# Optimization experiments

Hardware: AMD Instinct MI355X
Metric: run time of the kernel (lower is better)

The kernel has to match this reference:

```python
import jax, jax.numpy as jnp
import numpy as np

# ---- config (matches init_kwargs) ----
B, S, V = 8, 900, 11
H, NH, HD = 512, 8, 64          # hidden, heads, head_dim = H // NH
L = 2                            # num_layers
EXPANSION = 4.0
INNER = 1536                     # find_multiple(round(4.0 * 512 * 2/3), 256)
STEPS = 2                        # mcmc_num_steps
EPS = 1e-5                       # rms_norm_eps
THETA = 10000.0                  # rope_theta
ESCALE = float(np.sqrt(H))       # embed_scale = sqrt(hidden_size)
SCALE = 1.0 / float(np.sqrt(HD))


def rms_norm(x):
    return x * jax.lax.rsqrt(jnp.mean(x * x, axis=-1, keepdims=True) + EPS)


def rope_tables():
    inv_freq = 1.0 / (THETA ** (jnp.arange(0, HD, 2, dtype=jnp.float32) / HD))
    t = jnp.arange(S, dtype=jnp.float32)
    freqs = jnp.outer(t, inv_freq)                # (S, HD/2)
    emb = jnp.concatenate([freqs, freqs], axis=-1)  # (S, HD)
    return jnp.cos(emb), jnp.sin(emb)


def rotate_half(x):
    x1, x2 = jnp.split(x, 2, axis=-1)
    return jnp.concatenate([-x2, x1], axis=-1)


def apply_rope(q, k, cos, sin):
    cos = cos[None, :, None, :]  # (1,S,1,HD) broadcast over batch & heads
    sin = sin[None, :, None, :]
    return q * cos + rotate_half(q) * sin, k * cos + rotate_half(k) * sin


def block(h, qkv_w, o_w, gu_w, d_w, cos, sin):
    b, s, _ = h.shape
    qkv = (h @ qkv_w).reshape(b, s, 3 * NH, HD)
    q, k, v = qkv[:, :, :NH], qkv[:, :, NH:2 * NH], qkv[:, :, 2 * NH:]
    q, k = apply_rope(q, k, cos, sin)
    scores = jnp.einsum('bqhd,bkhd->bhqk', q, k) * SCALE
    attn = jax.nn.softmax(scores, axis=-1)
    out = jnp.einsum('bhqk,bkhd->bqhd', attn, v).reshape(b, s, NH * HD)
    h = rms_norm(h + out @ o_w)                   # post-norm residual
    gu = h @ gu_w
    gate, up = gu[..., :INNER], gu[..., INNER:]
    h = rms_norm(h + (jax.nn.silu(gate) * up) @ d_w)
    return h


def energy(logits, embed_w, energy_w, qkv_w, o_w, gu_w, d_w, input_emb, cos, sin):
    probs = jax.nn.softmax(logits, axis=-1)       # soft token distribution
    h = input_emb + ESCALE * (probs @ embed_w)    # soft embedding
    for i in range(L):
        h = block(h, qkv_w[i], o_w[i], gu_w[i], d_w[i], cos, sin)
    return jnp.sum(h @ energy_w)                  # scalar energy


def setup_inputs() -> dict:
    key = jax.random.key(0)
    ks = jax.random.split(key, 8)
    inputs = jax.random.randint(ks[0], (B, S), 0, V, dtype=jnp.int64)
    puzzle_identifiers = jax.random.randint(ks[1], (B,), 0, 1, dtype=jnp.int64)
    init_std = 1.0 / ESCALE
    embed_w = jax.random.normal(ks[2], (V, H), jnp.float32) * init_std
    energy_w = jax.random.normal(ks[3], (H, 1), jnp.float32) * 0.02
    qkv_w = jax.random.normal(ks[4], (L, H, 3 * NH * HD), jnp.float32) * 0.02
    o_w = jax.random.normal(ks[5], (L, NH * HD, H), jnp.float32) * 0.02
    gu_w = jax.random.normal(ks[6], (L, H, 2 * INNER), jnp.float32) * 0.02
    d_w = jax.random.normal(ks[7], (L, INNER, H), jnp.float32) * 0.02
    alpha = jnp.asarray(100.0, jnp.float32)       # mcmc_step_size
    return {"inputs": inputs, "puzzle_identifiers": puzzle_identifiers,
            "embed_w": embed_w, "energy_w": energy_w, "qkv_w": qkv_w,
            "o_w": o_w, "gu_w": gu_w, "d_w": d_w, "alpha": alpha}


def reference(inputs, puzzle_identifiers, embed_w, energy_w, qkv_w, o_w, gu_w, d_w, alpha):
    cos, sin = rope_tables()
    input_emb = ESCALE * embed_w[inputs]          # (B,S,H)
    a = jnp.maximum(alpha, 1e-4)                  # torch.clamp(alpha, min=1e-4)
    logits = jnp.zeros((inputs.shape[0], S, V), jnp.float32)
    egrad = jax.grad(energy)
    for _ in range(STEPS):                        # MCMC energy-descent loop
        g = egrad(logits, embed_w, energy_w, qkv_w, o_w, gu_w, d_w, input_emb, cos, sin)
        logits = logits - a * g
    return logits
```

## Files before the change

kernel.cpp:

```cpp
#include <hip/hip_runtime.h>
#include <math.h>

#define B_ 8
#define S_ 900
#define V_ 11
#define H_ 512
#define NH_ 8
#define HD_ 64
#define INNER_ 1536
#define STEPS_ 2
#define NTOK (B_*S_)
#define EPS_ 1e-5f
#define THETA_ 10000.0f
#define ESCALE_ 22.627416997969522f
#define SCALE_ 0.125f
#define PT_ 68

typedef __attribute__((ext_vector_type(8))) short bh8;
typedef __attribute__((ext_vector_type(4))) float f32x4;
typedef __attribute__((ext_vector_type(4))) unsigned short us4;

union bfu { bh8 v; unsigned short s[8]; us4 q[2]; };

__device__ inline unsigned short f2bf(float x) {
  unsigned u = __builtin_bit_cast(unsigned, x);
  return (unsigned short)((u + 0x7FFFu + ((u >> 16) & 1u)) >> 16);
}
__device__ inline float b2f(unsigned short s) {
  return __builtin_bit_cast(float, (unsigned)s << 16);
}

__device__ inline void gld16(const unsigned short* g, unsigned short* l) {
  __builtin_amdgcn_global_load_lds(
      (const __attribute__((address_space(1))) void*)(g),
      (__attribute__((address_space(3))) void*)(l), 16, 0, 0);
}

__device__ inline bh8 lds16(const unsigned short* p) {
  bfu u;
  u.q[0] = *(const us4*)p;
  u.q[1] = *(const us4*)(p + 4);
  return u.v;
}
__device__ inline void sts16(unsigned short* p, bfu u) {
  *(us4*)p = u.q[0];
  *(us4*)(p + 4) = u.q[1];
}

__device__ inline float wave_sum64(float x) {
#pragma unroll
  for (int off = 32; off > 0; off >>= 1) x += __shfl_xor(x, off, 64);
  return x;
}

__device__ inline float quad_sum(float x) {
  x += __shfl_xor(x, 1, 64);
  x += __shfl_xor(x, 2, 64);
  return x;
}


__global__ void k_zero(float* p, int n) {
  int i = blockIdx.x * blockDim.x + threadIdx.x;
  if (i < n) p[i] = 0.f;
}

__global__ void k_rope_tables(float* cs, float* sn) {
  int idx = blockIdx.x * blockDim.x + threadIdx.x;
  if (idx >= S_ * 32) return;
  int s = idx >> 5, i = idx & 31;
  float freq = powf(THETA_, -(float)i / 32.0f);
  float ang = (float)s * freq;
  cs[idx] = cosf(ang);
  sn[idx] = sinf(ang);
}

__global__ void k_softmax_logits(const float* __restrict__ logits, float* __restrict__ P) {
  int t = blockIdx.x * blockDim.x + threadIdx.x;
  if (t >= NTOK) return;
  float x[V_];
  float m = -1e30f;
#pragma unroll
  for (int v = 0; v < V_; ++v) { x[v] = logits[t * V_ + v]; m = fmaxf(m, x[v]); }
  float ssum = 0.f;
#pragma unroll
  for (int v = 0; v < V_; ++v) { x[v] = expf(x[v] - m); ssum += x[v]; }
  float inv = 1.f / ssum;
#pragma unroll
  for (int v = 0; v < V_; ++v) P[t * V_ + v] = x[v] * inv;
}

__global__ void k_h0(const float* __restrict__ P, const float* __restrict__ E,
                     const int* __restrict__ inp, float* __restrict__ h0,
                     unsigned short* __restrict__ h016) {
  int t = blockIdx.x;
  int tid = threadIdx.x;
  __shared__ float p[V_];
  __shared__ int iw;
  if (tid < V_) p[tid] = P[t * V_ + tid];
  if (tid == 0) iw = inp[t];
  __syncthreads();
  for (int h = tid; h < H_; h += blockDim.x) {
    float acc = E[iw * H_ + h];
#pragma unroll
    for (int v = 0; v < V_; ++v) acc += p[v] * E[v * H_ + h];
    float val = ESCALE_ * acc;
    h0[(size_t)t * H_ + h] = val;
    h016[(size_t)t * H_ + h] = f2bf(val);
  }
}

__global__ void k_gfill(const float* __restrict__ ew, float* __restrict__ G) {
  int idx = blockIdx.x * blockDim.x + threadIdx.x;
  if (idx < NTOK * H_) G[idx] = ew[idx & (H_ - 1)];
}

__global__ void k_cast8(const float* __restrict__ X, unsigned short* __restrict__ Y, int n8) {
  int i = blockIdx.x * blockDim.x + threadIdx.x;
  if (i >= n8) return;
  const float4* p = (const float4*)(X + (size_t)i * 8);
  float4 a = p[0], b = p[1];
  bfu o;
  o.s[0] = f2bf(a.x); o.s[1] = f2bf(a.y); o.s[2] = f2bf(a.z); o.s[3] = f2bf(a.w);
  o.s[4] = f2bf(b.x); o.s[5] = f2bf(b.y); o.s[6] = f2bf(b.z); o.s[7] = f2bf(b.w);
  *(bh8*)(Y + (size_t)i * 8) = o.v;
}


__global__ void k_wt(const float* __restrict__ W, unsigned short* __restrict__ WT, int K, int N) {
  __shared__ float t[32][33];
  int k0 = blockIdx.y * 32, n0 = blockIdx.x * 32;
  int tx = threadIdx.x, ty = threadIdx.y;
#pragma unroll
  for (int i = 0; i < 4; ++i)
    t[ty + 8 * i][tx] = W[(size_t)(k0 + ty + 8 * i) * N + n0 + tx];
  __syncthreads();
#pragma unroll
  for (int i = 0; i < 4; ++i)
    WT[(size_t)(n0 + ty + 8 * i) * K + k0 + tx] = f2bf(t[tx][ty + 8 * i]);
}


template <int SILU_A, int ADD, int CBF, int ROPE, int SILUBWD>
__global__ __launch_bounds__(256) void k_gemm(const unsigned short* __restrict__ A16,
                                              const unsigned short* __restrict__ Bt,
                                              const float* __restrict__ Dm,
                                              float* __restrict__ Cf,
                                              unsigned short* __restrict__ C16,
                                              unsigned short* __restrict__ GU,
                                              const float* __restrict__ Cs,
                                              const float* __restrict__ Sn,
                                              int M, int N, int K, int lda) {
  __shared__ unsigned short As[64][32];
  __shared__ unsigned short Bs[128][32];
  int tid = threadIdx.x;
  int m0 = blockIdx.y * 64, n0 = blockIdx.x * 128;
  int wid = tid >> 6, lane = tid & 63;
  int wr = (wid >> 1) * 32, wc = (wid & 1) * 64;
  int lr = lane & 15, lg = lane >> 4;
  int srow = lane >> 2, sck = (lane & 3) * 8;
  f32x4 acc[2][4] = {};
  for (int k0 = 0; k0 < K; k0 += 32) {
    __syncthreads();
    if (SILU_A) {
      int row = tid >> 2, ck = (tid & 3) * 8;
      int gr = m0 + row; gr = gr < M ? gr : M - 1;
      const unsigned short* src = &A16[(size_t)gr * lda + k0 + ck];
      bfu pa;
#pragma unroll
      for (int j = 0; j < 8; ++j) {
        float g = b2f(src[j]), u = b2f(src[INNER_ + j]);
        pa.s[j] = f2bf((g / (1.f + __expf(-g))) * u);
      }
      *(bh8*)&As[row][ck] = pa.v;
    } else {
      int row = wid * 16 + srow;
      int gr = m0 + row; gr = gr < M ? gr : M - 1;
      gld16(&A16[(size_t)gr * lda + k0 + sck], &As[wid * 16][0]);
    }
#pragma unroll
    for (int i = 0; i < 2; ++i) {
      int bb = wid * 2 + i;
      gld16(&Bt[(size_t)(n0 + bb * 16 + srow) * K + k0 + sck], &Bs[bb * 16][0]);
    }
    __syncthreads();
    bh8 av[2], bv[4];
#pragma unroll
    for (int fr = 0; fr < 2; ++fr) av[fr] = *(const bh8*)&As[wr + fr * 16 + lr][lg * 8];
#pragma unroll
    for (int fc = 0; fc < 4; ++fc) bv[fc] = *(const bh8*)&Bs[wc + fc * 16 + lr][lg * 8];
#pragma unroll
    for (int fr = 0; fr < 2; ++fr)
#pragma unroll
      for (int fc = 0; fc < 4; ++fc)
        acc[fr][fc] = __builtin_amdgcn_mfma_f32_16x16x32_bf16(av[fr], bv[fc], acc[fr][fc], 0, 0, 0);
  }
  bool rope_on = ROPE && (((n0 + wc) >> 6) < 16);
#pragma unroll
  for (int fr = 0; fr < 2; ++fr) {
    int r0 = m0 + wr + fr * 16 + lg * 4;
#pragma unroll
    for (int i = 0; i < 4; ++i) {
      int gr = r0 + i;
      if (gr >= M) continue;
      float c0 = 1.f, s0 = 0.f, c1 = 1.f, s1 = 0.f;
      if (ROPE) {
        if (rope_on) {
          int s = gr % S_;
          c0 = Cs[s * 32 + lr];      s0 = Sn[s * 32 + lr];
          c1 = Cs[s * 32 + 16 + lr]; s1 = Sn[s * 32 + 16 + lr];
        }
      }
#pragma unroll
      for (int fc = 0; fc < 4; ++fc) {
        int gc = n0 + wc + fc * 16 + lr;
        float out = acc[fr][fc][i];
        if (ROPE) {
          float part = acc[fr][fc ^ 2][i];
          float cc = (fc & 1) ? c1 : c0;
          float ss = (fc & 1) ? s1 : s0;
          out = (fc < 2) ? (out * cc - part * ss) : (out * cc + part * ss);
        }
        if (ADD) out += Dm[(size_t)gr * N + gc];
        if (SILUBWD) {
          size_t gb = (size_t)gr * (size_t)(2 * INNER_) + gc;
          float g = b2f(GU[gb]), u = b2f(GU[gb + INNER_]);
          float sig = 1.f / (1.f + __expf(-g));
          GU[gb] = f2bf(out * u * sig * (1.f + g * (1.f - sig)));
          GU[gb + INNER_] = f2bf(out * g * sig);
        } else if (CBF) {
          C16[(size_t)gr * N + gc] = f2bf(out);
        } else {
          Cf[(size_t)gr * N + gc] = out;
        }
      }
    }
  }
}


__global__ __launch_bounds__(256) void k_attn_fwd3(const unsigned short* __restrict__ QKV,
                                                   unsigned short* __restrict__ AO,
                                                   float* __restrict__ MB,
                                                   float* __restrict__ LB) {
  __shared__ unsigned short Ks[64][PT_];
  __shared__ unsigned short VT[64][PT_];
  __shared__ unsigned short Ps[4][16][PT_];
  int tid = threadIdx.x;
  int h = blockIdx.y, b = blockIdx.z;
  int w = tid >> 6, lane = tid & 63;
  int lr = lane & 15, lg = lane >> 4;
  int q0 = blockIdx.x * 64 + w * 16;

  bh8 qf[2];
  {
    int qr = q0 + lr; if (qr >= S_) qr = S_ - 1;
    const unsigned short* qp = &QKV[((size_t)(b * S_ + qr) * 24 + h) * 64 + lg * 8];
    qf[0] = *(const bh8*)qp;
    qf[1] = *(const bh8*)(qp + 32);
  }
  f32x4 accO[4] = {};
  float m[4], lsum[4];
#pragma unroll
  for (int i = 0; i < 4; ++i) { m[i] = -1e30f; lsum[i] = 0.f; }

  for (int kt = 0; kt < S_; kt += 64) {
    __syncthreads();
    {
      int r = tid >> 2, c0 = (tid & 3) * 16;
      int src = kt + r;
      size_t ts = (size_t)b * S_ + (src < S_ ? src : S_ - 1);
      const unsigned short* gp = &QKV[(ts * 24 + 8 + h) * 64 + c0];
      bfu p0, p1;
      p0.v = *(const bh8*)gp;
      p1.v = *(const bh8*)(gp + 8);
      sts16(&Ks[r][c0], p0);
      sts16(&Ks[r][c0 + 8], p1);
    }
    {
      int d0 = (tid & 15) * 4, k0r = (tid >> 4) * 4;
      us4 rv[4];
#pragma unroll
      for (int j = 0; j < 4; ++j) {
        int src = kt + k0r + j;
        size_t ts = (size_t)b * S_ + (src < S_ ? src : S_ - 1);
        rv[j] = *(const us4*)&QKV[(ts * 24 + 16 + h) * 64 + d0];
      }
#pragma unroll
      for (int dd = 0; dd < 4; ++dd) {
        us4 pk = {rv[0][dd], rv[1][dd], rv[2][dd], rv[3][dd]};
        *(us4*)&VT[d0 + dd][k0r] = pk;
      }
    }
    __syncthreads();
    f32x4 accS[4] = {};
#pragma unroll
    for (int ks = 0; ks < 2; ++ks)
#pragma unroll
      for (int fk = 0; fk < 4; ++fk)
        accS[fk] = __builtin_amdgcn_mfma_f32_16x16x32_bf16(qf[ks], lds16(&Ks[fk * 16 + lr][ks * 32 + lg * 8]), accS[fk], 0, 0, 0);
    float sc[4][4], pmax[4];
#pragma unroll
    for (int i = 0; i < 4; ++i) pmax[i] = -1e30f;
#pragma unroll
    for (int fk = 0; fk < 4; ++fk)
#pragma unroll
      for (int i = 0; i < 4; ++i) {
        float s = accS[fk][i] * SCALE_;
        if (kt + fk * 16 + lr >= S_) s = -1e30f;
        sc[fk][i] = s;
        pmax[i] = fmaxf(pmax[i], s);
      }
#pragma unroll
    for (int i = 0; i < 4; ++i) {
      float v = pmax[i];
      v = fmaxf(v, __shfl_xor(v, 1, 64));
      v = fmaxf(v, __shfl_xor(v, 2, 64));
      v = fmaxf(v, __shfl_xor(v, 4, 64));
      v = fmaxf(v, __shfl_xor(v, 8, 64));
      pmax[i] = v;
    }
    float psum[4];
#pragma unroll
    for (int i = 0; i < 4; ++i) {
      float mn = fmaxf(m[i], pmax[i]);
      float eo = __expf(m[i] - mn);
      m[i] = mn;
      lsum[i] *= eo;
#pragma unroll
      for (int fd = 0; fd < 4; ++fd) accO[fd][i] *= eo;
      psum[i] = 0.f;
    }
#pragma unroll
    for (int fk = 0; fk < 4; ++fk)
#pragma unroll
      for (int i = 0; i < 4; ++i) {
        float p = __expf(sc[fk][i] - m[i]);
        sc[fk][i] = p;
        psum[i] += p;
      }
#pragma unroll
    for (int i = 0; i < 4; ++i) {
      float v = psum[i];
      v += __shfl_xor(v, 1, 64);
      v += __shfl_xor(v, 2, 64);
      v += __shfl_xor(v, 4, 64);
      v += __shfl_xor(v, 8, 64);
      lsum[i] += v;
    }
#pragma unroll
    for (int fk = 0; fk < 4; ++fk)
#pragma unroll
      for (int i = 0; i < 4; ++i)
        Ps[w][lg * 4 + i][fk * 16 + lr] = f2bf(sc[fk][i]);
#pragma unroll
    for (int ks = 0; ks < 2; ++ks) {
      bh8 ap = lds16(&Ps[w][lr][ks * 32 + lg * 8]);
#pragma unroll
      for (int fd = 0; fd < 4; ++fd)
        accO[fd] = __builtin_amdgcn_mfma_f32_16x16x32_bf16(ap, lds16(&VT[fd * 16 + lr][ks * 32 + lg * 8]), accO[fd], 0, 0, 0);
    }
  }
#pragma unroll
  for (int i = 0; i < 4; ++i) {
    int q = q0 + lg * 4 + i;
    if (q < S_) {
      float linv = 1.f / lsum[i];
      size_t obase = (size_t)(b * S_ + q) * H_ + h * 64;
#pragma unroll
      for (int fd = 0; fd < 4; ++fd) AO[obase + fd * 16 + lr] = f2bf(accO[fd][i] * linv);
      if (lr == 0) {
        MB[((size_t)b * NH_ + h) * S_ + q] = m[i];
        LB[((size_t)b * NH_ + h) * S_ + q] = linv;
      }
    }
  }
}

__global__ __launch_bounds__(256) void k_delta(const unsigned short* __restrict__ O,
                                               const unsigned short* __restrict__ dO,
                                               float* __restrict__ DB) {
  int tid = threadIdx.x;
  int h = blockIdx.y, b = blockIdx.z;
  int r = blockIdx.x * 64 + (tid >> 2), part = tid & 3;
  if (r >= S_) return;
  size_t base = (size_t)(b * S_ + r) * H_ + h * 64 + part * 16;
  bfu o0, o1, d0, d1;
  o0.v = *(const bh8*)&O[base];  o1.v = *(const bh8*)&O[base + 8];
  d0.v = *(const bh8*)&dO[base]; d1.v = *(const bh8*)&dO[base + 8];
  float s = 0.f;
#pragma unroll
  for (int j = 0; j < 8; ++j)
    s += b2f(o0.s[j]) * b2f(d0.s[j]) + b2f(o1.s[j]) * b2f(d1.s[j]);
  s = quad_sum(s);
  if (part == 0) DB[((size_t)b * NH_ + h) * S_ + r] = s;
}

__global__ __launch_bounds__(256) void k_attn_bwd_dq3(const unsigned short* __restrict__ QKV,
                                                      const unsigned short* __restrict__ dO,
                                                      const float* __restrict__ MB,
                                                      const float* __restrict__ LB,
                                                      const float* __restrict__ DB,
                                                      const float* __restrict__ Cs,
                                                      const float* __restrict__ Sn,
                                                      unsigned short* __restrict__ dQKV) {
  __shared__ unsigned short Ks[64][PT_];
  __shared__ unsigned short Vs[64][PT_];
  __shared__ unsigned short KT[64][PT_];
  __shared__ unsigned short Ps[4][16][PT_];
  int tid = threadIdx.x;
  int h = blockIdx.y, b = blockIdx.z;
  int w = tid >> 6, lane = tid & 63;
  int lr = lane & 15, lg = lane >> 4;
  int q0 = blockIdx.x * 64 + w * 16;
  size_t sbase = ((size_t)b * NH_ + h) * S_;

  bh8 qf[2], dof[2];
  {
    int qr = q0 + lr; if (qr >= S_) qr = S_ - 1;
    const unsigned short* qp = &QKV[((size_t)(b * S_ + qr) * 24 + h) * 64 + lg * 8];
    const unsigned short* dp = &dO[(size_t)(b * S_ + qr) * H_ + h * 64 + lg * 8];
    qf[0] = *(const bh8*)qp;  qf[1] = *(const bh8*)(qp + 32);
    dof[0] = *(const bh8*)dp; dof[1] = *(const bh8*)(dp + 32);
  }
  float mrow[4], lrow[4], drow[4];
#pragma unroll
  for (int i = 0; i < 4; ++i) {
    int q = q0 + lg * 4 + i; if (q >= S_) q = S_ - 1;
    mrow[i] = MB[sbase + q];
    lrow[i] = LB[sbase + q];
    drow[i] = DB[sbase + q];
  }
  f32x4 accQ[4] = {};

  for (int kt = 0; kt < S_; kt += 64) {
    __syncthreads();
    {
      int r = tid >> 2, c0 = (tid & 3) * 16;
      int src = kt + r;
      bool vld = src < S_;
      size_t ts = (size_t)b * S_ + (vld ? src : S_ - 1);
      const unsigned short* kp = &QKV[(ts * 24 + 8 + h) * 64 + c0];
      bfu p0{}, p1{}, p2{}, p3{};
      if (vld) {
        p0.v = *(const bh8*)kp;
        p1.v = *(const bh8*)(kp + 8);
        p2.v = *(const bh8*)(kp + 512);
        p3.v = *(const bh8*)(kp + 520);
      }
      sts16(&Ks[r][c0], p0); sts16(&Ks[r][c0 + 8], p1);
      sts16(&Vs[r][c0], p2); sts16(&Vs[r][c0 + 8], p3);
    }
    {
      int d0 = (tid & 15) * 4, k0r = (tid >> 4) * 4;
      us4 rv[4];
#pragma unroll
      for (int j = 0; j < 4; ++j) {
        int src = kt + k0r + j;
        bool vld = src < S_;
        size_t ts = (size_t)b * S_ + (vld ? src : S_ - 1);
        us4 t = *(const us4*)&QKV[(ts * 24 + 8 + h) * 64 + d0];
        if (!vld) t = us4{0, 0, 0, 0};
        rv[j] = t;
      }
#pragma unroll
      for (int dd = 0; dd < 4; ++dd) {
        us4 pk = {rv[0][dd], rv[1][dd], rv[2][dd], rv[3][dd]};
        *(us4*)&KT[d0 + dd][k0r] = pk;
      }
    }
    __syncthreads();
    f32x4 aS[4] = {}, aD[4] = {};
#pragma unroll
    for (int ks = 0; ks < 2; ++ks)
#pragma unroll
      for (int fk = 0; fk < 4; ++fk) {
        aS[fk] = __builtin_amdgcn_mfma_f32_16x16x32_bf16(qf[ks], lds16(&Ks[fk * 16 + lr][ks * 32 + lg * 8]), aS[fk], 0, 0, 0);
        aD[fk] = __builtin_amdgcn_mfma_f32_16x16x32_bf16(dof[ks], lds16(&Vs[fk * 16 + lr][ks * 32 + lg * 8]), aD[fk], 0, 0, 0);
      }
#pragma unroll
    for (int fk = 0; fk < 4; ++fk)
#pragma unroll
      for (int i = 0; i < 4; ++i) {
        float p = __expf(aS[fk][i] * SCALE_ - mrow[i]) * lrow[i];
        float ds = p * (aD[fk][i] - drow[i]);
        Ps[w][lg * 4 + i][fk * 16 + lr] = f2bf(ds);
      }
#pragma unroll
    for (int ks = 0; ks < 2; ++ks) {
      bh8 ap = lds16(&Ps[w][lr][ks * 32 + lg * 8]);
#pragma unroll
      for (int fd = 0; fd < 4; ++fd)
        accQ[fd] = __builtin_amdgcn_mfma_f32_16x16x32_bf16(ap, lds16(&KT[fd * 16 + lr][ks * 32 + lg * 8]), accQ[fd], 0, 0, 0);
    }
  }
#pragma unroll
  for (int i = 0; i < 4; ++i) {
    int q = q0 + lg * 4 + i;
    if (q < S_) {
      size_t obase = ((size_t)(b * S_ + q) * 24 + h) * 64;
      float c0 = Cs[q * 32 + lr], s0 = Sn[q * 32 + lr];
      float c1 = Cs[q * 32 + 16 + lr], s1 = Sn[q * 32 + 16 + lr];
#pragma unroll
      for (int fd = 0; fd < 4; ++fd) {
        float x = SCALE_ * accQ[fd][i];
        float p = SCALE_ * accQ[fd ^ 2][i];
        float cc = (fd & 1) ? c1 : c0;
        float ss = (fd & 1) ? s1 : s0;
        float out = (fd < 2) ? (x * cc + p * ss) : (x * cc - p * ss);
        dQKV[obase + fd * 16 + lr] = f2bf(out);
      }
    }
  }
}

__global__ __launch_bounds__(256) void k_attn_bwd_kv3(const unsigned short* __restrict__ QKV,
                                                      const unsigned short* __restrict__ dO,
                                                      const float* __restrict__ MB,
                                                      const float* __restrict__ LB,
                                                      const float* __restrict__ DB,
                                                      const float* __restrict__ Cs,
                                                      const float* __restrict__ Sn,
                                                      unsigned short* __restrict__ dQKV) {
  __shared__ unsigned short Qs[64][PT_];
  __shared__ unsigned short dOs[64][PT_];
  __shared__ unsigned short QT[64][PT_];
  __shared__ unsigned short dOT[64][PT_];
  __shared__ unsigned short Ps[4][16][PT_];
  __shared__ float sM[64], sL[64], sD[64];
  int tid = threadIdx.x;
  int h = blockIdx.y, b = blockIdx.z;
  int w = tid >> 6, lane = tid & 63;
  int lr = lane & 15, lg = lane >> 4;
  int k0w = blockIdx.x * 64 + w * 16;
  size_t sbase = ((size_t)b * NH_ + h) * S_;

  bh8 kf[2], vf[2];
  {
    int kr = k0w + lr; if (kr >= S_) kr = S_ - 1;
    const unsigned short* kp = &QKV[((size_t)(b * S_ + kr) * 24 + 8 + h) * 64 + lg * 8];
    kf[0] = *(const bh8*)kp;        kf[1] = *(const bh8*)(kp + 32);
    vf[0] = *(const bh8*)(kp + 512); vf[1] = *(const bh8*)(kp + 544);
  }
  f32x4 accK[4] = {}, accV[4] = {};

  for (int qt = 0; qt < S_; qt += 64) {
    __syncthreads();
    {
      int r = tid >> 2, c0 = (tid & 3) * 16;
      int src = qt + r;
      bool vld = src < S_;
      size_t ts = (size_t)b * S_ + (vld ? src : S_ - 1);
      const unsigned short* qp = &QKV[(ts * 24 + h) * 64 + c0];
      const unsigned short* dp = &dO[ts * H_ + h * 64 + c0];
      bfu p0, p1, p2{}, p3{};
      p0.v = *(const bh8*)qp;
      p1.v = *(const bh8*)(qp + 8);
      if (vld) {
        p2.v = *(const bh8*)dp;
        p3.v = *(const bh8*)(dp + 8);
      }
      sts16(&Qs[r][c0], p0);  sts16(&Qs[r][c0 + 8], p1);
      sts16(&dOs[r][c0], p2); sts16(&dOs[r][c0 + 8], p3);
    }
    {
      int d0 = (tid & 15) * 4, q0r = (tid >> 4) * 4;
      us4 rq[4], rd[4];
#pragma unroll
      for (int j = 0; j < 4; ++j) {
        int src = qt + q0r + j;
        bool vld = src < S_;
        size_t ts = (size_t)b * S_ + (vld ? src : S_ - 1);
        rq[j] = *(const us4*)&QKV[(ts * 24 + h) * 64 + d0];
        us4 td = *(const us4*)&dO[ts * H_ + h * 64 + d0];
        if (!vld) td = us4{0, 0, 0, 0};
        rd[j] = td;
      }
#pragma unroll
      for (int dd = 0; dd < 4; ++dd) {
        us4 pq = {rq[0][dd], rq[1][dd], rq[2][dd], rq[3][dd]};
        us4 pd = {rd[0][dd], rd[1][dd], rd[2][dd], rd[3][dd]};
        *(us4*)&QT[d0 + dd][q0r] = pq;
        *(us4*)&dOT[d0 + dd][q0r] = pd;
      }
    }
    if (tid < 64) {
      int src = qt + tid;
      bool vld = src < S_;
      int sc = vld ? src : S_ - 1;
      sM[tid] = MB[sbase + sc];
      sL[tid] = LB[sbase + sc];
      sD[tid] = vld ? DB[sbase + sc] : 0.f;
    }
    __syncthreads();
    f32x4 aS[4] = {}, aD[4] = {};
#pragma unroll
    for (int ks = 0; ks < 2; ++ks)
#pragma unroll
      for (int fq = 0; fq < 4; ++fq) {
        aS[fq] = __builtin_amdgcn_mfma_f32_16x16x32_bf16(kf[ks], lds16(&Qs[fq * 16 + lr][ks * 32 + lg * 8]), aS[fq], 0, 0, 0);
        aD[fq] = __builtin_amdgcn_mfma_f32_16x16x32_bf16(vf[ks], lds16(&dOs[fq * 16 + lr][ks * 32 + lg * 8]), aD[fq], 0, 0, 0);
      }
    float pv[4][4];
#pragma unroll
    for (int fq = 0; fq < 4; ++fq) {
      float mq = sM[fq * 16 + lr], lq = sL[fq * 16 + lr];
#pragma unroll
      for (int i = 0; i < 4; ++i) {
        float p = __expf(aS[fq][i] * SCALE_ - mq) * lq;
        pv[fq][i] = p;
        Ps[w][lg * 4 + i][fq * 16 + lr] = f2bf(p);
      }
    }
#pragma unroll
    for (int qs = 0; qs < 2; ++qs) {
      bh8 ap = lds16(&Ps[w][lr][qs * 32 + lg * 8]);
#pragma unroll
      for (int fd = 0; fd < 4; ++fd)
        accV[fd] = __builtin_amdgcn_mfma_f32_16x16x32_bf16(ap, lds16(&dOT[fd * 16 + lr][qs * 32 + lg * 8]), accV[fd], 0, 0, 0);
    }
#pragma unroll
    for (int fq = 0; fq < 4; ++fq) {
      float dq = sD[fq * 16 + lr];
#pragma unroll
      for (int i = 0; i < 4; ++i)
        Ps[w][lg * 4 + i][fq * 16 + lr] = f2bf(pv[fq][i] * (aD[fq][i] - dq));
    }
#pragma unroll
    for (int qs = 0; qs < 2; ++qs) {
      bh8 ap = lds16(&Ps[w][lr][qs * 32 + lg * 8]);
#pragma unroll
      for (int fd = 0; fd < 4; ++fd)
        accK[fd] = __builtin_amdgcn_mfma_f32_16x16x32_bf16(ap, lds16(&QT[fd * 16 + lr][qs * 32 + lg * 8]), accK[fd], 0, 0, 0);
    }
  }
#pragma unroll
  for (int i = 0; i < 4; ++i) {
    int k = k0w + lg * 4 + i;
    if (k < S_) {
      size_t obase = ((size_t)(b * S_ + k) * 24 + 8 + h) * 64;
      float c0 = Cs[k * 32 + lr], s0 = Sn[k * 32 + lr];
      float c1 = Cs[k * 32 + 16 + lr], s1 = Sn[k * 32 + 16 + lr];
#pragma unroll
      for (int fd = 0; fd < 4; ++fd) {
        float x = SCALE_ * accK[fd][i];
        float p = SCALE_ * accK[fd ^ 2][i];
        float cc = (fd & 1) ? c1 : c0;
        float ss = (fd & 1) ? s1 : s0;
        float out = (fd < 2) ? (x * cc + p * ss) : (x * cc - p * ss);
        dQKV[obase + fd * 16 + lr] = f2bf(out);
        dQKV[obase + 512 + fd * 16 + lr] = f2bf(accV[fd][i]);
      }
    }
  }
}


__global__ __launch_bounds__(256) void k_rms_fwd(const float* __restrict__ X, float* __restrict__ Y,
                                                 unsigned short* __restrict__ Y16) {
  int t = blockIdx.x, tid = threadIdx.x;
  float x0 = X[(size_t)t * H_ + tid], x1 = X[(size_t)t * H_ + tid + 256];
  __shared__ float red[256];
  red[tid] = x0 * x0 + x1 * x1;
  __syncthreads();
  for (int s = 128; s > 0; s >>= 1) {
    if (tid < s) red[tid] += red[tid + s];
    __syncthreads();
  }
  float r = rsqrtf(red[0] / H_ + EPS_);
  float y0 = x0 * r, y1 = x1 * r;
  Y[(size_t)t * H_ + tid] = y0;
  Y[(size_t)t * H_ + tid + 256] = y1;
  Y16[(size_t)t * H_ + tid] = f2bf(y0);
  Y16[(size_t)t * H_ + tid + 256] = f2bf(y1);
}

__global__ __launch_bounds__(256) void k_rms_bwd(const float* __restrict__ X,
                                                 const float* __restrict__ GY,
                                                 float* __restrict__ GX,
                                                 unsigned short* __restrict__ GX16) {
  int t = blockIdx.x, tid = threadIdx.x;
  float x0 = X[(size_t)t * H_ + tid], x1 = X[(size_t)t * H_ + tid + 256];
  float g0 = GY[(size_t)t * H_ + tid], g1 = GY[(size_t)t * H_ + tid + 256];
  __shared__ float r1[256], r2[256];
  r1[tid] = x0 * x0 + x1 * x1;
  r2[tid] = x0 * g0 + x1 * g1;
  __syncthreads();
  for (int s = 128; s > 0; s >>= 1) {
    if (tid < s) { r1[tid] += r1[tid + s]; r2[tid] += r2[tid + s]; }
    __syncthreads();
  }
  float r = rsqrtf(r1[0] / H_ + EPS_);
  float coef = r * r * r * r2[0] / (float)H_;
  float o0 = r * g0 - coef * x0, o1 = r * g1 - coef * x1;
  GX[(size_t)t * H_ + tid] = o0;
  GX[(size_t)t * H_ + tid + 256] = o1;
  GX16[(size_t)t * H_ + tid] = f2bf(o0);
  GX16[(size_t)t * H_ + tid + 256] = f2bf(o1);
}


__global__ __launch_bounds__(64) void k_logits_update(const float* __restrict__ G,
                                                      const float* __restrict__ E,
                                                      const float* __restrict__ P,
                                                      const float* __restrict__ alpha,
                                                      float* __restrict__ logits) {
  int t = blockIdx.x, lane = threadIdx.x;
  float dp[V_];
#pragma unroll
  for (int v = 0; v < V_; ++v) dp[v] = 0.f;
  for (int hh = lane; hh < H_; hh += 64) {
    float gh = G[(size_t)t * H_ + hh];
#pragma unroll
    for (int v = 0; v < V_; ++v) dp[v] += gh * E[v * H_ + hh];
  }
#pragma unroll
  for (int v = 0; v < V_; ++v) dp[v] = wave_sum64(dp[v]) * ESCALE_;
  float dot = 0.f;
  float pv[V_];
#pragma unroll
  for (int v = 0; v < V_; ++v) {
    pv[v] = P[t * V_ + v];
    dot += pv[v] * dp[v];
  }
  float a = fmaxf(alpha[0], 1e-4f);
  if (lane < V_) logits[t * V_ + lane] -= a * pv[lane] * (dp[lane] - dot);
}


struct Ctx {
  unsigned short *Q16, *Q016, *dQ16, *GU16, *DO16, *AO16, *AO016, *X116, *UDX16;
  float *X1, *X2, *G, *UDX, *P, *MB, *LB, *DB, *MB0, *LB0, *CS, *SN;
  const unsigned short *WTqkv[2], *WTo[2], *WTgu[2], *WTd[2];
  const unsigned short *WSqkv[2], *WSo[2], *WSgu[2], *WSd[2];
  hipStream_t st;
};

static inline dim3 ggrid(int M, int N) { return dim3(N / 128, (M + 63) / 64); }

static void block_forward(Ctx& c, int l, const float* hin, const unsigned short* hin16,
                          float* hout, unsigned short* qb, unsigned short* ao,
                          float* mb, float* lb, bool skip_attn) {
  if (!skip_attn) {
    k_gemm<0, 0, 1, 1, 0><<<ggrid(NTOK, 3 * H_), 256, 0, c.st>>>(
        hin16, c.WTqkv[l], nullptr, nullptr, qb, nullptr, c.CS, c.SN, NTOK, 3 * H_, H_, H_);
    k_attn_fwd3<<<dim3((S_ + 63) / 64, NH_, B_), 256, 0, c.st>>>(qb, ao, mb, lb);
  }
  k_gemm<0, 1, 0, 0, 0><<<ggrid(NTOK, H_), 256, 0, c.st>>>(
      ao, c.WTo[l], hin, c.X1, nullptr, nullptr, nullptr, nullptr, NTOK, H_, H_, H_);
  k_rms_fwd<<<NTOK, 256, 0, c.st>>>(c.X1, c.UDX, c.UDX16);
  k_gemm<0, 0, 1, 0, 0><<<ggrid(NTOK, 2 * INNER_), 256, 0, c.st>>>(
      c.UDX16, c.WTgu[l], nullptr, nullptr, c.GU16, nullptr, nullptr, nullptr, NTOK, 2 * INNER_, H_, H_);
  k_gemm<1, 1, 0, 0, 0><<<ggrid(NTOK, H_), 256, 0, c.st>>>(
      c.GU16, c.WTd[l], c.UDX, c.X2, nullptr, nullptr, nullptr, nullptr, NTOK, H_, INNER_, 2 * INNER_);
  if (hout) k_rms_fwd<<<NTOK, 256, 0, c.st>>>(c.X2, hout, c.UDX16);
}

static void block_backward(Ctx& c, int l, const float* hin, const unsigned short* hin16,
                           unsigned short* qb, unsigned short* ao, float* mb, float* lb,
                           bool skip_attn) {
  block_forward(c, l, hin, hin16, nullptr, qb, ao, mb, lb, skip_attn);
  k_rms_bwd<<<NTOK, 256, 0, c.st>>>(c.X2, c.G, c.UDX, c.UDX16);
  k_gemm<0, 0, 0, 0, 1><<<ggrid(NTOK, INNER_), 256, 0, c.st>>>(
      c.UDX16, c.WSd[l], nullptr, nullptr, nullptr, c.GU16, nullptr, nullptr, NTOK, INNER_, H_, H_);
  k_gemm<0, 1, 0, 0, 0><<<ggrid(NTOK, H_), 256, 0, c.st>>>(
      c.GU16, c.WSgu[l], c.UDX, c.G, nullptr, nullptr, nullptr, nullptr, NTOK, H_, 2 * INNER_, 2 * INNER_);
  k_rms_bwd<<<NTOK, 256, 0, c.st>>>(c.X1, c.G, c.UDX, c.UDX16);
  k_gemm<0, 0, 1, 0, 0><<<ggrid(NTOK, H_), 256, 0, c.st>>>(
      c.UDX16, c.WSo[l], nullptr, nullptr, c.DO16, nullptr, nullptr, nullptr, NTOK, H_, H_, H_);
  dim3 agrid((S_ + 63) / 64, NH_, B_);
  k_delta<<<agrid, 256, 0, c.st>>>(ao, c.DO16, c.DB);
  k_attn_bwd_dq3<<<agrid, 256, 0, c.st>>>(qb, c.DO16, mb, lb, c.DB, c.CS, c.SN, c.dQ16);
  k_attn_bwd_kv3<<<agrid, 256, 0, c.st>>>(qb, c.DO16, mb, lb, c.DB, c.CS, c.SN, c.dQ16);
  k_gemm<0, 1, 0, 0, 0><<<ggrid(NTOK, H_), 256, 0, c.st>>>(
      c.dQ16, c.WSqkv[l], c.UDX, c.G, nullptr, nullptr, nullptr, nullptr, NTOK, H_, 3 * H_, 3 * H_);
}

extern "C" void kernel_launch(void* const* d_in, const int* in_sizes, int n_in,
                              void* d_out, int out_size, void* d_ws, size_t ws_size,
                              hipStream_t stream) {
  const int* inputs = (const int*)d_in[0];
  const float* E = (const float*)d_in[2];
  const float* ew = (const float*)d_in[3];
  const float* qkvw = (const float*)d_in[4];
  const float* ow = (const float*)d_in[5];
  const float* guw = (const float*)d_in[6];
  const float* dw = (const float*)d_in[7];
  const float* alpha = (const float*)d_in[8];
  float* logits = (float*)d_out;

  const size_t WT_FLOATS = 3407872;
  const size_t NEED =
      3 * ((size_t)NTOK * 3 * H_ / 2) +
      ((size_t)NTOK * INNER_) +
      4 * ((size_t)NTOK * H_) +
      5 * ((size_t)NTOK * H_ / 2) +
      ((size_t)NTOK * V_) +
      5 * ((size_t)B_ * NH_ * S_) +
      2 * ((size_t)S_ * 32) +
      2 * WT_FLOATS;
  if (ws_size < NEED * sizeof(float)) {
    k_zero<<<(NTOK * V_ + 255) / 256, 256, 0, stream>>>(logits, NTOK * V_);
    return;
  }

  float* f = (float*)d_ws;
  Ctx c;
  c.st = stream;
  c.Q16 = (unsigned short*)f;  f += (size_t)NTOK * 3 * H_ / 2;
  c.Q016 = (unsigned short*)f; f += (size_t)NTOK * 3 * H_ / 2;
  c.dQ16 = (unsigned short*)f; f += (size_t)NTOK * 3 * H_ / 2;
  c.GU16 = (unsigned short*)f; f += (size_t)NTOK * INNER_;
  c.X1 = f;   f += (size_t)NTOK * H_;
  c.X2 = f;   f += (size_t)NTOK * H_;
  c.G = f;    f += (size_t)NTOK * H_;
  c.UDX = f;  f += (size_t)NTOK * H_;
  c.AO16 = (unsigned short*)f;  f += (size_t)NTOK * H_ / 2;
  c.AO016 = (unsigned short*)f; f += (size_t)NTOK * H_ / 2;
  c.DO16 = (unsigned short*)f;  f += (size_t)NTOK * H_ / 2;
  c.X116 = (unsigned short*)f;  f += (size_t)NTOK * H_ / 2;
  c.UDX16 = (unsigned short*)f; f += (size_t)NTOK * H_ / 2;
  c.P = f;    f += (size_t)NTOK * V_;
  c.MB = f;   f += (size_t)B_ * NH_ * S_;
  c.LB = f;   f += (size_t)B_ * NH_ * S_;
  c.DB = f;   f += (size_t)B_ * NH_ * S_;
  c.MB0 = f;  f += (size_t)B_ * NH_ * S_;
  c.LB0 = f;  f += (size_t)B_ * NH_ * S_;
  c.CS = f;   f += (size_t)S_ * 32;
  c.SN = f;   f += (size_t)S_ * 32;
  unsigned short* wt = (unsigned short*)f;

  const size_t LQKV = (size_t)H_ * 3 * H_;
  const size_t LO = (size_t)H_ * H_;
  const size_t LGU = (size_t)H_ * 2 * INNER_;
  const size_t LD = (size_t)INNER_ * H_;

  for (int l = 0; l < 2; ++l) {
    c.WTqkv[l] = wt;
    k_wt<<<dim3(3 * H_ / 32, H_ / 32), dim3(32, 8), 0, stream>>>(qkvw + l * LQKV, wt, H_, 3 * H_);
    wt += LQKV;
    c.WTo[l] = wt;
    k_wt<<<dim3(H_ / 32, H_ / 32), dim3(32, 8), 0, stream>>>(ow + l * LO, wt, H_, H_);
    wt += LO;
    c.WTgu[l] = wt;
    k_wt<<<dim3(2 * INNER_ / 32, H_ / 32), dim3(32, 8), 0, stream>>>(guw + l * LGU, wt, H_, 2 * INNER_);
    wt += LGU;
    c.WTd[l] = wt;
    k_wt<<<dim3(H_ / 32, INNER_ / 32), dim3(32, 8), 0, stream>>>(dw + l * LD, wt, INNER_, H_);
    wt += LD;
  }
  {
    unsigned short* ws = wt;
    k_cast8<<<(int)((2 * LQKV / 8 + 255) / 256), 256, 0, stream>>>(qkvw, ws, (int)(2 * LQKV / 8));
    c.WSqkv[0] = ws; c.WSqkv[1] = ws + LQKV; ws += 2 * LQKV;
    k_cast8<<<(int)((2 * LO / 8 + 255) / 256), 256, 0, stream>>>(ow, ws, (int)(2 * LO / 8));
    c.WSo[0] = ws; c.WSo[1] = ws + LO; ws += 2 * LO;
    k_cast8<<<(int)((2 * LGU / 8 + 255) / 256), 256, 0, stream>>>(guw, ws, (int)(2 * LGU / 8));
    c.WSgu[0] = ws; c.WSgu[1] = ws + LGU; ws += 2 * LGU;
    k_cast8<<<(int)((2 * LD / 8 + 255) / 256), 256, 0, stream>>>(dw, ws, (int)(2 * LD / 8));
    c.WSd[0] = ws; c.WSd[1] = ws + LD;
  }

  k_zero<<<(NTOK * V_ + 255) / 256, 256, 0, stream>>>(logits, NTOK * V_);
  k_rope_tables<<<(S_ * 32 + 255) / 256, 256, 0, stream>>>(c.CS, c.SN);

  for (int step = 0; step < STEPS_; ++step) {
    k_softmax_logits<<<(NTOK + 255) / 256, 256, 0, stream>>>(logits, c.P);
    k_h0<<<NTOK, 256, 0, stream>>>(c.P, E, inputs, c.X1, c.X116);
    block_forward(c, 0, c.X1, c.X116, c.UDX, c.Q016, c.AO016, c.MB0, c.LB0, false);
    k_gfill<<<(NTOK * H_ + 255) / 256, 256, 0, stream>>>(ew, c.G);
    block_backward(c, 1, c.UDX, c.UDX16, c.Q16, c.AO16, c.MB, c.LB, false);
    k_h0<<<NTOK, 256, 0, stream>>>(c.P, E, inputs, c.X1, c.X116);
    block_backward(c, 0, c.X1, c.X116, c.Q016, c.AO016, c.MB0, c.LB0, true);
    k_logits_update<<<NTOK, 64, 0, stream>>>(c.G, E, c.P, alpha, logits);
  }
}
```

Baseline: 2.635 ms.

## Add 128-row GEMM tiles and cache layer-0 forward activations for backward recompute

Adds a TM template parameter to the bf16 MFMA GEMM so the wide-N GEMMs (QKV, gate/up, SiLU-backward) use 128x128 tiles for more reuse per block. Layer 0's forward now keeps its post-MLP residual (X20) and normalized bf16 input (U016). Layer 0's backward therefore skips the rms_fwd and down-projection recompute. The O-projection and gate/up GEMMs are still rerun, since X1 and GU16 get overwritten by layer 1. This costs two extra workspace buffers and more accumulator registers per thread in the 128-row tiles.

```diff
diff --git a/kernel.cpp b/kernel.cpp
--- a/kernel.cpp
+++ b/kernel.cpp
@@ -141,7 +141,7 @@
 }
 
 
-template <int SILU_A, int ADD, int CBF, int ROPE, int SILUBWD>
+template <int TM, int SILU_A, int ADD, int CBF, int ROPE, int SILUBWD>
 __global__ __launch_bounds__(256) void k_gemm(const unsigned short* __restrict__ A16,
                                               const unsigned short* __restrict__ Bt,
                                               const float* __restrict__ Dm,
@@ -151,32 +151,36 @@
                                               const float* __restrict__ Cs,
                                               const float* __restrict__ Sn,
                                               int M, int N, int K, int lda) {
-  __shared__ unsigned short As[64][32];
+  __shared__ unsigned short As[TM][32];
   __shared__ unsigned short Bs[128][32];
+  constexpr int FR = TM / 32;
   int tid = threadIdx.x;
-  int m0 = blockIdx.y * 64, n0 = blockIdx.x * 128;
+  int m0 = blockIdx.y * TM, n0 = blockIdx.x * 128;
   int wid = tid >> 6, lane = tid & 63;
-  int wr = (wid >> 1) * 32, wc = (wid & 1) * 64;
+  int wr = (wid >> 1) * (FR * 16), wc = (wid & 1) * 64;
   int lr = lane & 15, lg = lane >> 4;
   int srow = lane >> 2, sck = (lane & 3) * 8;
-  f32x4 acc[2][4] = {};
+  f32x4 acc[FR][4] = {};
   for (int k0 = 0; k0 < K; k0 += 32) {
     __syncthreads();
-    if (SILU_A) {
-      int row = tid >> 2, ck = (tid & 3) * 8;
-      int gr = m0 + row; gr = gr < M ? gr : M - 1;
-      const unsigned short* src = &A16[(size_t)gr * lda + k0 + ck];
-      bfu pa;
-#pragma unroll
-      for (int j = 0; j < 8; ++j) {
-        float g = b2f(src[j]), u = b2f(src[INNER_ + j]);
-        pa.s[j] = f2bf((g / (1.f + __expf(-g))) * u);
-      }
-      *(bh8*)&As[row][ck] = pa.v;
-    } else {
-      int row = wid * 16 + srow;
-      int gr = m0 + row; gr = gr < M ? gr : M - 1;
-      gld16(&A16[(size_t)gr * lda + k0 + sck], &As[wid * 16][0]);
+#pragma unroll
+    for (int half = 0; half < TM / 64; ++half) {
+      if (SILU_A) {
+        int row = (tid >> 2) + 64 * half;
+        int ck = (tid & 3) * 8;
+        int gr = m0 + row; gr = gr < M ? gr : M - 1;
+        const unsigned short* src = &A16[(size_t)gr * lda + k0 + ck];
+        bfu pa;
+#pragma unroll
+        for (int j = 0; j < 8; ++j) {
+          float g = b2f(src[j]), u = b2f(src[INNER_ + j]);
+          pa.s[j] = f2bf((g / (1.f + __expf(-g))) * u);
+        }
+        *(bh8*)&As[row][ck] = pa.v;
+      } else {
+        int gr = m0 + 64 * half + wid * 16 + srow; gr = gr < M ? gr : M - 1;
+        gld16(&A16[(size_t)gr * lda + k0 + sck], &As[64 * half + wid * 16][0]);
+      }
     }
 #pragma unroll
     for (int i = 0; i < 2; ++i) {
@@ -184,20 +188,20 @@
       gld16(&Bt[(size_t)(n0 + bb * 16 + srow) * K + k0 + sck], &Bs[bb * 16][0]);
     }
     __syncthreads();
-    bh8 av[2], bv[4];
-#pragma unroll
-    for (int fr = 0; fr < 2; ++fr) av[fr] = *(const bh8*)&As[wr + fr * 16 + lr][lg * 8];
+    bh8 av[FR], bv[4];
+#pragma unroll
+    for (int fr = 0; fr < FR; ++fr) av[fr] = *(const bh8*)&As[wr + fr * 16 + lr][lg * 8];
 #pragma unroll
     for (int fc = 0; fc < 4; ++fc) bv[fc] = *(const bh8*)&Bs[wc + fc * 16 + lr][lg * 8];
 #pragma unroll
-    for (int fr = 0; fr < 2; ++fr)
+    for (int fr = 0; fr < FR; ++fr)
 #pragma unroll
       for (int fc = 0; fc < 4; ++fc)
         acc[fr][fc] = __builtin_amdgcn_mfma_f32_16x16x32_bf16(av[fr], bv[fc], acc[fr][fc], 0, 0, 0);
   }
   bool rope_on = ROPE && (((n0 + wc) >> 6) < 16);
 #pragma unroll
-  for (int fr = 0; fr < 2; ++fr) {
+  for (int fr = 0; fr < FR; ++fr) {
     int r0 = m0 + wr + fr * 16 + lg * 4;
 #pragma unroll
     for (int i = 0; i < 4; ++i) {
@@ -729,50 +733,56 @@
 
 
 struct Ctx {
-  unsigned short *Q16, *Q016, *dQ16, *GU16, *DO16, *AO16, *AO016, *X116, *UDX16;
-  float *X1, *X2, *G, *UDX, *P, *MB, *LB, *DB, *MB0, *LB0, *CS, *SN;
+  unsigned short *Q16, *Q016, *dQ16, *GU16, *DO16, *AO16, *AO016, *X116, *UDX16, *U016;
+  float *X1, *X2, *X20, *G, *UDX, *P, *MB, *LB, *DB, *MB0, *LB0, *CS, *SN;
   const unsigned short *WTqkv[2], *WTo[2], *WTgu[2], *WTd[2];
   const unsigned short *WSqkv[2], *WSo[2], *WSgu[2], *WSd[2];
   hipStream_t st;
 };
 
-static inline dim3 ggrid(int M, int N) { return dim3(N / 128, (M + 63) / 64); }
-
 static void block_forward(Ctx& c, int l, const float* hin, const unsigned short* hin16,
                           float* hout, unsigned short* qb, unsigned short* ao,
-                          float* mb, float* lb, bool skip_attn) {
-  if (!skip_attn) {
-    k_gemm<0, 0, 1, 1, 0><<<ggrid(NTOK, 3 * H_), 256, 0, c.st>>>(
-        hin16, c.WTqkv[l], nullptr, nullptr, qb, nullptr, c.CS, c.SN, NTOK, 3 * H_, H_, H_);
-    k_attn_fwd3<<<dim3((S_ + 63) / 64, NH_, B_), 256, 0, c.st>>>(qb, ao, mb, lb);
-  }
-  k_gemm<0, 1, 0, 0, 0><<<ggrid(NTOK, H_), 256, 0, c.st>>>(
+                          float* mb, float* lb, float* x2buf, unsigned short* u16buf) {
+  k_gemm<128, 0, 0, 1, 1, 0><<<dim3(3 * H_ / 128, (NTOK + 127) / 128), 256, 0, c.st>>>(
+      hin16, c.WTqkv[l], nullptr, nullptr, qb, nullptr, c.CS, c.SN, NTOK, 3 * H_, H_, H_);
+  k_attn_fwd3<<<dim3((S_ + 63) / 64, NH_, B_), 256, 0, c.st>>>(qb, ao, mb, lb);
+  k_gemm<64, 0, 1, 0, 0, 0><<<dim3(H_ / 128, (NTOK + 63) / 64), 256, 0, c.st>>>(
       ao, c.WTo[l], hin, c.X1, nullptr, nullptr, nullptr, nullptr, NTOK, H_, H_, H_);
-  k_rms_fwd<<<NTOK, 256, 0, c.st>>>(c.X1, c.UDX, c.UDX16);
-  k_gemm<0, 0, 1, 0, 0><<<ggrid(NTOK, 2 * INNER_), 256, 0, c.st>>>(
-      c.UDX16, c.WTgu[l], nullptr, nullptr, c.GU16, nullptr, nullptr, nullptr, NTOK, 2 * INNER_, H_, H_);
-  k_gemm<1, 1, 0, 0, 0><<<ggrid(NTOK, H_), 256, 0, c.st>>>(
-      c.GU16, c.WTd[l], c.UDX, c.X2, nullptr, nullptr, nullptr, nullptr, NTOK, H_, INNER_, 2 * INNER_);
-  if (hout) k_rms_fwd<<<NTOK, 256, 0, c.st>>>(c.X2, hout, c.UDX16);
+  k_rms_fwd<<<NTOK, 256, 0, c.st>>>(c.X1, c.UDX, u16buf);
+  k_gemm<128, 0, 0, 1, 0, 0><<<dim3(2 * INNER_ / 128, (NTOK + 127) / 128), 256, 0, c.st>>>(
+      u16buf, c.WTgu[l], nullptr, nullptr, c.GU16, nullptr, nullptr, nullptr, NTOK, 2 * INNER_, H_, H_);
+  k_gemm<64, 1, 1, 0, 0, 0><<<dim3(H_ / 128, (NTOK + 63) / 64), 256, 0, c.st>>>(
+      c.GU16, c.WTd[l], c.UDX, x2buf, nullptr, nullptr, nullptr, nullptr, NTOK, H_, INNER_, 2 * INNER_);
+  if (hout) k_rms_fwd<<<NTOK, 256, 0, c.st>>>(x2buf, hout, c.UDX16);
 }
 
 static void block_backward(Ctx& c, int l, const float* hin, const unsigned short* hin16,
                            unsigned short* qb, unsigned short* ao, float* mb, float* lb,
-                           bool skip_attn) {
-  block_forward(c, l, hin, hin16, nullptr, qb, ao, mb, lb, skip_attn);
-  k_rms_bwd<<<NTOK, 256, 0, c.st>>>(c.X2, c.G, c.UDX, c.UDX16);
-  k_gemm<0, 0, 0, 0, 1><<<ggrid(NTOK, INNER_), 256, 0, c.st>>>(
+                           bool full) {
+  const float* x2src;
+  if (full) {
+    block_forward(c, l, hin, hin16, nullptr, qb, ao, mb, lb, c.X2, c.UDX16);
+    x2src = c.X2;
+  } else {
+    k_gemm<64, 0, 1, 0, 0, 0><<<dim3(H_ / 128, (NTOK + 63) / 64), 256, 0, c.st>>>(
+        ao, c.WTo[l], hin, c.X1, nullptr, nullptr, nullptr, nullptr, NTOK, H_, H_, H_);
+    k_gemm<128, 0, 0, 1, 0, 0><<<dim3(2 * INNER_ / 128, (NTOK + 127) / 128), 256, 0, c.st>>>(
+        c.U016, c.WTgu[l], nullptr, nullptr, c.GU16, nullptr, nullptr, nullptr, NTOK, 2 * INNER_, H_, H_);
+    x2src = c.X20;
+  }
+  k_rms_bwd<<<NTOK, 256, 0, c.st>>>(x2src, c.G, c.UDX, c.UDX16);
+  k_gemm<128, 0, 0, 0, 0, 1><<<dim3(INNER_ / 128, (NTOK + 127) / 128), 256, 0, c.st>>>(
       c.UDX16, c.WSd[l], nullptr, nullptr, nullptr, c.GU16, nullptr, nullptr, NTOK, INNER_, H_, H_);
-  k_gemm<0, 1, 0, 0, 0><<<ggrid(NTOK, H_), 256, 0, c.st>>>(
+  k_gemm<64, 0, 1, 0, 0, 0><<<dim3(H_ / 128, (NTOK + 63) / 64), 256, 0, c.st>>>(
       c.GU16, c.WSgu[l], c.UDX, c.G, nullptr, nullptr, nullptr, nullptr, NTOK, H_, 2 * INNER_, 2 * INNER_);
   k_rms_bwd<<<NTOK, 256, 0, c.st>>>(c.X1, c.G, c.UDX, c.UDX16);
-  k_gemm<0, 0, 1, 0, 0><<<ggrid(NTOK, H_), 256, 0, c.st>>>(
+  k_gemm<64, 0, 0, 1, 0, 0><<<dim3(H_ / 128, (NTOK + 63) / 64), 256, 0, c.st>>>(
       c.UDX16, c.WSo[l], nullptr, nullptr, c.DO16, nullptr, nullptr, nullptr, NTOK, H_, H_, H_);
   dim3 agrid((S_ + 63) / 64, NH_, B_);
   k_delta<<<agrid, 256, 0, c.st>>>(ao, c.DO16, c.DB);
   k_attn_bwd_dq3<<<agrid, 256, 0, c.st>>>(qb, c.DO16, mb, lb, c.DB, c.CS, c.SN, c.dQ16);
   k_attn_bwd_kv3<<<agrid, 256, 0, c.st>>>(qb, c.DO16, mb, lb, c.DB, c.CS, c.SN, c.dQ16);
-  k_gemm<0, 1, 0, 0, 0><<<ggrid(NTOK, H_), 256, 0, c.st>>>(
+  k_gemm<64, 0, 1, 0, 0, 0><<<dim3(H_ / 128, (NTOK + 63) / 64), 256, 0, c.st>>>(
       c.dQ16, c.WSqkv[l], c.UDX, c.G, nullptr, nullptr, nullptr, nullptr, NTOK, H_, 3 * H_, 3 * H_);
 }
 
@@ -793,8 +803,8 @@
   const size_t NEED =
       3 * ((size_t)NTOK * 3 * H_ / 2) +
       ((size_t)NTOK * INNER_) +
-      4 * ((size_t)NTOK * H_) +
-      5 * ((size_t)NTOK * H_ / 2) +
+      5 * ((size_t)NTOK * H_) +
+      6 * ((size_t)NTOK * H_ / 2) +
       ((size_t)NTOK * V_) +
       5 * ((size_t)B_ * NH_ * S_) +
       2 * ((size_t)S_ * 32) +
@@ -813,6 +823,7 @@
   c.GU16 = (unsigned short*)f; f += (size_t)NTOK * INNER_;
   c.X1 = f;   f += (size_t)NTOK * H_;
   c.X2 = f;   f += (size_t)NTOK * H_;
+  c.X20 = f;  f += (size_t)NTOK * H_;
   c.G = f;    f += (size_t)NTOK * H_;
   c.UDX = f;  f += (size_t)NTOK * H_;
   c.AO16 = (unsigned short*)f;  f += (size_t)NTOK * H_ / 2;
@@ -820,6 +831,7 @@
   c.DO16 = (unsigned short*)f;  f += (size_t)NTOK * H_ / 2;
   c.X116 = (unsigned short*)f;  f += (size_t)NTOK * H_ / 2;
   c.UDX16 = (unsigned short*)f; f += (size_t)NTOK * H_ / 2;
+  c.U016 = (unsigned short*)f;  f += (size_t)NTOK * H_ / 2;
   c.P = f;    f += (size_t)NTOK * V_;
   c.MB = f;   f += (size_t)B_ * NH_ * S_;
   c.LB = f;   f += (size_t)B_ * NH_ * S_;
@@ -867,11 +879,11 @@
   for (int step = 0; step < STEPS_; ++step) {
     k_softmax_logits<<<(NTOK + 255) / 256, 256, 0, stream>>>(logits, c.P);
     k_h0<<<NTOK, 256, 0, stream>>>(c.P, E, inputs, c.X1, c.X116);
-    block_forward(c, 0, c.X1, c.X116, c.UDX, c.Q016, c.AO016, c.MB0, c.LB0, false);
+    block_forward(c, 0, c.X1, c.X116, c.UDX, c.Q016, c.AO016, c.MB0, c.LB0, c.X20, c.U016);
     k_gfill<<<(NTOK * H_ + 255) / 256, 256, 0, stream>>>(ew, c.G);
-    block_backward(c, 1, c.UDX, c.UDX16, c.Q16, c.AO16, c.MB, c.LB, false);
+    block_backward(c, 1, c.UDX, c.UDX16, c.Q16, c.AO16, c.MB, c.LB, true);
     k_h0<<<NTOK, 256, 0, stream>>>(c.P, E, inputs, c.X1, c.X116);
-    block_backward(c, 0, c.X1, c.X116, c.Q016, c.AO016, c.MB0, c.LB0, true);
+    block_backward(c, 0, c.X1, c.X116, c.Q016, c.AO016, c.MB0, c.LB0, false);
     k_logits_update<<<NTOK, 64, 0, stream>>>(c.G, E, c.P, alpha, logits);
   }
 }
```

Measured after the change: 2.430 ms. 7.8% less time.
